# Kernel optimization log

Measured on AMD Instinct MI355X. Metric: run time of the kernel, lower is better.

Reference implementation:

```python
import jax, jax.numpy as jnp
import numpy as np
import math

N_HEADS = 16
ROPE_THETA = 10000.0


def _rope_cos_sin(seqlen, head_dim, theta=ROPE_THETA):
    # freqs_cis = polar(1, outer(t, 1/theta^(2i/d))) -> return cos, sin parts
    inv = 1.0 / (theta ** (jnp.arange(0, head_dim, 2, dtype=jnp.float32) / head_dim))
    t = jnp.arange(seqlen, dtype=jnp.float32)
    freqs = t[:, None] * inv[None, :]          # [S, hd/2]
    return jnp.cos(freqs), jnp.sin(freqs)


def _apply_rope(x, cos, sin):
    # x: [B, S, H, hd]; treat consecutive pairs as complex, rotate by e^{i*freq}
    B, S, H, hd = x.shape
    x2 = x.astype(jnp.float32).reshape(B, S, H, hd // 2, 2)
    xr, xi = x2[..., 0], x2[..., 1]
    c = cos[None, :, None, :]
    s = sin[None, :, None, :]
    out_r = xr * c - xi * s
    out_i = xr * s + xi * c
    return jnp.stack([out_r, out_i], axis=-1).reshape(B, S, H, hd).astype(x.dtype)


def setup_inputs() -> dict:
    key = jax.random.key(0)
    ks = jax.random.split(key, 5)
    dim = 2048
    B, S = 2, 2048
    scale = 1.0 / math.sqrt(dim)
    x = jax.random.normal(ks[0], (B, S, dim), dtype=jnp.float32)
    wq = jax.random.normal(ks[1], (dim, dim), dtype=jnp.float32) * scale
    wk = jax.random.normal(ks[2], (dim, dim), dtype=jnp.float32) * scale
    wv = jax.random.normal(ks[3], (dim, dim), dtype=jnp.float32) * scale
    wo = jax.random.normal(ks[4], (dim, dim), dtype=jnp.float32) * scale
    return {"x": x, "wq": wq, "wk": wk, "wv": wv, "wo": wo}


def reference(x, wq, wk, wv, wo):
    B, S, D = x.shape
    H = N_HEADS
    hd = D // H
    # nn.Linear(bias=False): y = x @ W.T
    q = (x @ wq.T).reshape(B, S, H, hd)
    k = (x @ wk.T).reshape(B, S, H, hd)
    v = (x @ wv.T).reshape(B, S, H, hd)
    cos, sin = _rope_cos_sin(S, hd)
    q = _apply_rope(q, cos, sin)
    k = _apply_rope(k, cos, sin)
    attn = jnp.einsum('bthd,bThd->bhtT', q, k) / jnp.sqrt(jnp.float32(hd))
    attn = jax.nn.softmax(attn, axis=-1)
    out = jnp.einsum('bhtT,bThd->bthd', attn, v).reshape(B, S, D)
    return out @ wo.T
```

## Files before the change

kernel.cpp:

```cpp
#include <hip/hip_runtime.h>
#include <math.h>

typedef unsigned short u16;
typedef __bf16 bf16x8 __attribute__((ext_vector_type(8)));
typedef short s16x4 __attribute__((ext_vector_type(4)));
typedef short s16x8 __attribute__((ext_vector_type(8)));
typedef float f32x4 __attribute__((ext_vector_type(4)));

#define B_ 2
#define S_ 2048
#define D_ 2048
#define H_ 16
#define HD_ 128
#define M_ 4096
#define N3_ 6144

#define AS1(p) ((__attribute__((address_space(1))) void*)(void*)(p))
#define AS3(p) ((__attribute__((address_space(3))) void*)(p))
#define GLD16(g, l) __builtin_amdgcn_global_load_lds(AS1(g), AS3(l), 16, 0, 0)

__device__ __forceinline__ u16 f2bf(float f) {
  unsigned u = __float_as_uint(f);
  return (u16)((u + 0x7FFFu + ((u >> 16) & 1u)) >> 16);
}
__device__ __forceinline__ float bf2f(u16 v) {
  return __uint_as_float(((unsigned)v) << 16);
}

__global__ void cvt5_k(const float* __restrict__ x, const float* __restrict__ wq,
                       const float* __restrict__ wk, const float* __restrict__ wv,
                       const float* __restrict__ wo, u16* __restrict__ xb,
                       u16* __restrict__ wqkvb, u16* __restrict__ wob) {
  int y = blockIdx.y;
  const float* s;
  u16* d;
  int n4;
  if (y == 0) {
    s = x; d = xb; n4 = M_ * D_ / 4;
  } else {
    s = (y == 1) ? wq : (y == 2) ? wk : (y == 3) ? wv : wo;
    d = (y == 4) ? wob : wqkvb + (size_t)(y - 1) * D_ * D_;
    n4 = D_ * D_ / 4;
  }
  int i = blockIdx.x * 256 + threadIdx.x;
  if (i >= n4) return;
  float4 v = ((const float4*)s)[i];
  ushort4 o;
  o.x = f2bf(v.x); o.y = f2bf(v.y); o.z = f2bf(v.z); o.w = f2bf(v.w);
  ((ushort4*)d)[i] = o;
}

__global__ void rope_tab_k(float2* __restrict__ tab) {
  int t = blockIdx.x * 256 + threadIdx.x;
  if (t >= S_ * 64) return;
  int s = t >> 6, i = t & 63;
  double inv = exp2(-(double)i * (13.287712379549449 / 64.0));
  double fr = (double)s * inv;
  double sv, cv;
  sincos(fr, &sv, &cv);
  tab[t] = make_float2((float)cv, (float)sv);
}

template <typename OT>
__global__ __launch_bounds__(512, 2) void gemm256_k(const u16* __restrict__ A,
                                                    const u16* __restrict__ B,
                                                    OT* __restrict__ C,
                                                    int M, int N, int K) {
  __shared__ alignas(16) u16 sm[65536];
  const int tid = threadIdx.x;
  const int wid = tid >> 6, lane = tid & 63;
  const int quad = lane >> 4, l16 = lane & 15;
  const int wr = wid >> 2, wc = wid & 3;

  const int nby = M >> 8, nbx = N >> 8, nwg = nbx * nby;
  int bid = blockIdx.x;
  int wg = (nwg % 8 == 0) ? (bid % 8) * (nwg >> 3) + (bid >> 3) : bid;
  const int m0 = (wg % nby) << 8, n0 = (wg / nby) << 8;

  const int rr = tid >> 3;
  const int sw8 = ((tid & 7) ^ (rr & 7)) * 8;
  const int gb0 = (rr & 31) + ((rr & 32) << 1);
  const u16* pA0_0 = A + (size_t)(m0 + rr) * K + sw8;
  const u16* pA0_1 = A + (size_t)(m0 + 128 + rr) * K + sw8;
  const u16* pA1_0 = A + (size_t)(m0 + 64 + rr) * K + sw8;
  const u16* pA1_1 = A + (size_t)(m0 + 192 + rr) * K + sw8;
  const u16* pB0_0 = B + (size_t)(n0 + gb0) * K + sw8;
  const u16* pB0_1 = B + (size_t)(n0 + 128 + gb0) * K + sw8;
  const u16* pB1_0 = B + (size_t)(n0 + 32 + gb0) * K + sw8;
  const u16* pB1_1 = B + (size_t)(n0 + 160 + gb0) * K + sw8;
  const int dst0 = wid * 64 * 8, dst1 = (512 + wid * 64) * 8;

  const int pj0 = (quad ^ (l16 & 7)) * 8;
  const int pj1 = ((4 + quad) ^ (l16 & 7)) * 8;

  f32x4 acc[8][4] = {};
  const int NT = K >> 6;

  GLD16(pA0_0, sm + dst0);
  GLD16(pA0_1, sm + dst1);
  GLD16(pB0_0, sm + 32768 + dst0);
  GLD16(pB0_1, sm + 32768 + dst1);
  GLD16(pB1_0, sm + 32768 + 8192 + dst0);
  GLD16(pB1_1, sm + 32768 + 8192 + dst1);
  GLD16(pA1_0, sm + 8192 + dst0);
  GLD16(pA1_1, sm + 8192 + dst1);
  asm volatile("s_waitcnt vmcnt(4)" ::: "memory");
  asm volatile("s_barrier" ::: "memory");

  int koff = 0;
#pragma unroll 1
  for (int t = 0; t < NT; ++t) {
    const int aB = (t & 1) * 16384, bB = 32768 + (t & 1) * 16384;
    const int aN = ((t + 1) & 1) * 16384, bN = 32768 + ((t + 1) & 1) * 16384;
    const bool pre = (t + 1 < NT);
    const int kn = koff + 64;
    bf16x8 a_[4][2], b_[4][2];

#pragma unroll
    for (int m = 0; m < 4; ++m) {
      int rb = aB + (wr * 64 + m * 16 + l16) * 64;
      a_[m][0] = *(const bf16x8*)&sm[rb + pj0];
      a_[m][1] = *(const bf16x8*)&sm[rb + pj1];
    }
#pragma unroll
    for (int n = 0; n < 2; ++n) {
      int rb = bB + (wc * 32 + n * 16 + l16) * 64;
      b_[n][0] = *(const bf16x8*)&sm[rb + pj0];
      b_[n][1] = *(const bf16x8*)&sm[rb + pj1];
    }
    if (pre) { GLD16(pA0_0 + kn, sm + aN + dst0); GLD16(pA0_1 + kn, sm + aN + dst1); }
    asm volatile("s_barrier" ::: "memory");
    __builtin_amdgcn_s_setprio(1);
#pragma unroll
    for (int m = 0; m < 4; ++m)
#pragma unroll
      for (int n = 0; n < 2; ++n) {
        acc[m][n] = __builtin_amdgcn_mfma_f32_16x16x32_bf16(a_[m][0], b_[n][0], acc[m][n], 0, 0, 0);
        acc[m][n] = __builtin_amdgcn_mfma_f32_16x16x32_bf16(a_[m][1], b_[n][1], acc[m][n], 0, 0, 0);
      }
    __builtin_amdgcn_s_setprio(0);
    if (pre) asm volatile("s_waitcnt vmcnt(4)" ::: "memory");
    else     asm volatile("s_waitcnt vmcnt(0)" ::: "memory");
    asm volatile("s_barrier" ::: "memory");

#pragma unroll
    for (int n = 0; n < 2; ++n) {
      int rb = bB + (128 + wc * 32 + n * 16 + l16) * 64;
      b_[2 + n][0] = *(const bf16x8*)&sm[rb + pj0];
      b_[2 + n][1] = *(const bf16x8*)&sm[rb + pj1];
    }
    if (pre) { GLD16(pB0_0 + kn, sm + bN + dst0); GLD16(pB0_1 + kn, sm + bN + dst1); }
    asm volatile("s_barrier" ::: "memory");
    __builtin_amdgcn_s_setprio(1);
#pragma unroll
    for (int m = 0; m < 4; ++m)
#pragma unroll
      for (int n = 0; n < 2; ++n) {
        acc[m][2 + n] = __builtin_amdgcn_mfma_f32_16x16x32_bf16(a_[m][0], b_[2 + n][0], acc[m][2 + n], 0, 0, 0);
        acc[m][2 + n] = __builtin_amdgcn_mfma_f32_16x16x32_bf16(a_[m][1], b_[2 + n][1], acc[m][2 + n], 0, 0, 0);
      }
    __builtin_amdgcn_s_setprio(0);
    if (pre) asm volatile("s_waitcnt vmcnt(4)" ::: "memory");
    else     asm volatile("s_waitcnt vmcnt(0)" ::: "memory");
    asm volatile("s_barrier" ::: "memory");

#pragma unroll
    for (int m = 0; m < 4; ++m) {
      int rb = aB + (128 + wr * 64 + m * 16 + l16) * 64;
      a_[m][0] = *(const bf16x8*)&sm[rb + pj0];
      a_[m][1] = *(const bf16x8*)&sm[rb + pj1];
    }
    if (pre) { GLD16(pB1_0 + kn, sm + bN + 8192 + dst0); GLD16(pB1_1 + kn, sm + bN + 8192 + dst1); }
    asm volatile("s_barrier" ::: "memory");
    __builtin_amdgcn_s_setprio(1);
#pragma unroll
    for (int m = 0; m < 4; ++m)
#pragma unroll
      for (int n = 0; n < 2; ++n) {
        acc[4 + m][n] = __builtin_amdgcn_mfma_f32_16x16x32_bf16(a_[m][0], b_[n][0], acc[4 + m][n], 0, 0, 0);
        acc[4 + m][n] = __builtin_amdgcn_mfma_f32_16x16x32_bf16(a_[m][1], b_[n][1], acc[4 + m][n], 0, 0, 0);
      }
    __builtin_amdgcn_s_setprio(0);
    asm volatile("s_barrier" ::: "memory");

    if (pre) { GLD16(pA1_0 + kn, sm + aN + 8192 + dst0); GLD16(pA1_1 + kn, sm + aN + 8192 + dst1); }
    asm volatile("s_barrier" ::: "memory");
    __builtin_amdgcn_s_setprio(1);
#pragma unroll
    for (int m = 0; m < 4; ++m)
#pragma unroll
      for (int n = 0; n < 2; ++n) {
        acc[4 + m][2 + n] = __builtin_amdgcn_mfma_f32_16x16x32_bf16(a_[m][0], b_[2 + n][0], acc[4 + m][2 + n], 0, 0, 0);
        acc[4 + m][2 + n] = __builtin_amdgcn_mfma_f32_16x16x32_bf16(a_[m][1], b_[2 + n][1], acc[4 + m][2 + n], 0, 0, 0);
      }
    __builtin_amdgcn_s_setprio(0);
    asm volatile("s_waitcnt vmcnt(4)" ::: "memory");
    asm volatile("s_barrier" ::: "memory");
    koff = kn;
  }

#pragma unroll
  for (int m = 0; m < 8; ++m) {
#pragma unroll
    for (int n = 0; n < 4; ++n) {
      int col = n0 + wc * 64 + n * 16 + l16;
#pragma unroll
      for (int r = 0; r < 4; ++r) {
        int row = m0 + wr * 128 + m * 16 + quad * 4 + r;
        if constexpr (sizeof(OT) == 4)
          C[(size_t)row * N + col] = acc[m][n][r];
        else
          C[(size_t)row * N + col] = f2bf(acc[m][n][r]);
      }
    }
  }
}

template <typename OT>
__global__ __launch_bounds__(256) void gemm_bt_k(const u16* __restrict__ A,
                                                 const u16* __restrict__ B,
                                                 OT* __restrict__ C,
                                                 int M, int N, int K) {
  __shared__ alignas(16) u16 As[128 * 32];
  __shared__ alignas(16) u16 Bs[128 * 32];
  const int tid = threadIdx.x;
  const int wave = tid >> 6, lane = tid & 63;
  const int quad = lane >> 4, l16 = lane & 15;
  const int m0 = blockIdx.y * 128, n0 = blockIdx.x * 128;
  const int wm = (wave >> 1) * 64, wn = (wave & 1) * 64;
  const u16* Ag = A + (size_t)m0 * K;
  const u16* Bg = B + (size_t)n0 * K;
  f32x4 acc[4][4] = {};
  const int c0 = tid, c1 = tid + 256;
  const int r0 = c0 >> 2, k0b = (c0 & 3) * 8;
  const int r1 = c1 >> 2, k1b = (c1 & 3) * 8;
  u16* la0 = As + (size_t)(wave * 64) * 8;
  u16* la1 = As + (size_t)(256 + wave * 64) * 8;
  u16* lb0 = Bs + (size_t)(wave * 64) * 8;
  u16* lb1 = Bs + (size_t)(256 + wave * 64) * 8;
  for (int kt = 0; kt < K; kt += 32) {
    GLD16(Ag + (size_t)r0 * K + kt + k0b, la0);
    GLD16(Ag + (size_t)r1 * K + kt + k1b, la1);
    GLD16(Bg + (size_t)r0 * K + kt + k0b, lb0);
    GLD16(Bg + (size_t)r1 * K + kt + k1b, lb1);
    __syncthreads();
    bf16x8 af[4], bfr[4];
#pragma unroll
    for (int i = 0; i < 4; ++i)
      af[i] = *(const bf16x8*)&As[(wm + i * 16 + l16) * 32 + quad * 8];
#pragma unroll
    for (int j = 0; j < 4; ++j)
      bfr[j] = *(const bf16x8*)&Bs[(wn + j * 16 + l16) * 32 + quad * 8];
#pragma unroll
    for (int i = 0; i < 4; ++i)
#pragma unroll
      for (int j = 0; j < 4; ++j)
        acc[i][j] = __builtin_amdgcn_mfma_f32_16x16x32_bf16(af[i], bfr[j], acc[i][j], 0, 0, 0);
    __syncthreads();
  }
#pragma unroll
  for (int i = 0; i < 4; ++i) {
#pragma unroll
    for (int j = 0; j < 4; ++j) {
      int n = n0 + wn + j * 16 + l16;
#pragma unroll
      for (int r = 0; r < 4; ++r) {
        int m = m0 + wm + i * 16 + quad * 4 + r;
        if constexpr (sizeof(OT) == 4)
          C[(size_t)m * N + n] = acc[i][j][r];
        else
          C[(size_t)m * N + n] = f2bf(acc[i][j][r]);
      }
    }
  }
}

__global__ void rope_k(const u16* __restrict__ qkv, const float2* __restrict__ tab,
                       u16* __restrict__ Qr, u16* __restrict__ Kr) {
  int t = blockIdx.x * 256 + threadIdx.x;
  int m = t >> 10;
  int h = (t >> 6) & 15;
  int i = t & 63;
  int s = m & (S_ - 1);
  int b = m >> 11;
  float2 cs = tab[(s << 6) | i];
  const u16* qp = qkv + (size_t)m * N3_ + h * HD_ + 2 * i;
  ushort2 qv = *(const ushort2*)qp;
  ushort2 kv = *(const ushort2*)(qp + D_);
  float qr = bf2f(qv.x), qi = bf2f(qv.y);
  float kr = bf2f(kv.x), ki = bf2f(kv.y);
  ushort2 qo, ko;
  qo.x = f2bf(qr * cs.x - qi * cs.y);
  qo.y = f2bf(qr * cs.y + qi * cs.x);
  ko.x = f2bf(kr * cs.x - ki * cs.y);
  ko.y = f2bf(kr * cs.y + ki * cs.x);
  size_t o = ((size_t)(b * H_ + h) * S_ + s) * HD_ + 2 * i;
  *(ushort2*)(Qr + o) = qo;
  *(ushort2*)(Kr + o) = ko;
}

__global__ __launch_bounds__(256) void vperm_k(const u16* __restrict__ qkv,
                                               u16* __restrict__ Vp) {
  int bh = blockIdx.y;
  int b = bh >> 4, h = bh & 15;
  int t = blockIdx.x * 256 + threadIdx.x;
  int d = t & 127, g = t >> 7;
  const u16* src = qkv + ((size_t)(b * S_ + 4 * g)) * N3_ + 2 * D_ + h * HD_ + d;
  ushort4 o;
  o.x = src[0];
  o.y = src[N3_];
  o.z = src[2 * N3_];
  o.w = src[3 * N3_];
  *(ushort4*)(Vp + (size_t)bh * S_ * HD_ + (size_t)t * 4) = o;
}

#if __has_builtin(__builtin_amdgcn_mfma_f32_16x16x16bf16_1k)
#define HAS_MFMA16 1
#endif

__global__ __launch_bounds__(256, 2) void flash_k(const u16* __restrict__ Q,
                                                  const u16* __restrict__ Kc,
                                                  const u16* __restrict__ Vp,
                                                  u16* __restrict__ O) {
  __shared__ alignas(16) u16 sm[32768];
  const int tid = threadIdx.x;
  const int wave = tid >> 6, lane = tid & 63;
  const int quad = lane >> 4, l16 = lane & 15;
  const int qt = blockIdx.x, bh = blockIdx.y;
  const int b = bh >> 4, h = bh & 15;
  const u16* vbase_g = Vp + (size_t)bh * S_ * HD_;

#pragma unroll
  for (int i = 0; i < 8; ++i) {
    int c = i * 256 + tid, row = c >> 4, jl = c & 15;
    int gj = (jl & 8) | ((jl ^ row) & 7);
    GLD16(Q + ((size_t)bh * S_ + qt * 128 + row) * HD_ + gj * 8,
          sm + (size_t)(i * 256 + wave * 64) * 8);
  }
#pragma unroll
  for (int i = 0; i < 4; ++i) {
    int c = i * 256 + tid, row = c >> 4, jl = c & 15;
    int gj = (jl & 8) | ((jl ^ row) & 7);
    GLD16(Kc + ((size_t)bh * S_ + row) * HD_ + gj * 8,
          sm + 16384 + (size_t)(i * 256 + wave * 64) * 8);
    GLD16(vbase_g + (size_t)(i * 256 + tid) * 8,
          sm + 24576 + (size_t)(i * 256 + wave * 64) * 8);
  }
  __syncthreads();

  bf16x8 qf[2][4];
#pragma unroll
  for (int qs = 0; qs < 2; ++qs) {
    int row = wave * 32 + qs * 16 + l16;
#pragma unroll
    for (int dk = 0; dk < 4; ++dk) {
      int c = dk * 4 + quad, pj = (c & 8) | ((c ^ row) & 7);
      qf[qs][dk] = *(const bf16x8*)&sm[row * 128 + pj * 8];
    }
  }
  __syncthreads();

  f32x4 acco[2][8] = {};
  f32x4 accl[2] = {};
  const float SCL = 0.08838834764831845f * 1.4426950408889634f;
#ifdef HAS_MFMA16
  const s16x4 ones = {(short)0x3F80, (short)0x3F80, (short)0x3F80, (short)0x3F80};
#else
  union { s16x8 s; bf16x8 b; } onesu;
  onesu.s = (s16x8){(short)0x3F80, (short)0x3F80, (short)0x3F80, (short)0x3F80,
                    (short)0x3F80, (short)0x3F80, (short)0x3F80, (short)0x3F80};
#endif

#pragma unroll 1
  for (int kt = 0; kt < 32; ++kt) {
    u16* cb = sm + ((kt & 1) ? 0 : 16384);
    u16* nb = sm + ((kt & 1) ? 16384 : 0);
    if (kt < 31) {
      const u16* vg = vbase_g + (size_t)(kt + 1) * 8192;
#pragma unroll
      for (int i = 0; i < 4; ++i) {
        int c = i * 256 + tid, row = c >> 4, jl = c & 15;
        int gj = (jl & 8) | ((jl ^ row) & 7);
        GLD16(Kc + ((size_t)bh * S_ + (kt + 1) * 64 + row) * HD_ + gj * 8,
              nb + (size_t)(i * 256 + wave * 64) * 8);
        GLD16(vg + (size_t)(i * 256 + tid) * 8,
              nb + 8192 + (size_t)(i * 256 + wave * 64) * 8);
      }
    }

    f32x4 sc[2][4] = {};
#pragma unroll
    for (int k4 = 0; k4 < 4; ++k4) {
      int row = k4 * 16 + l16;
#pragma unroll
      for (int dk = 0; dk < 4; ++dk) {
        int c = dk * 4 + quad, pj = (c & 8) | ((c ^ row) & 7);
        bf16x8 kf = *(const bf16x8*)&cb[row * 128 + pj * 8];
        sc[0][k4] = __builtin_amdgcn_mfma_f32_16x16x32_bf16(kf, qf[0][dk], sc[0][k4], 0, 0, 0);
        sc[1][k4] = __builtin_amdgcn_mfma_f32_16x16x32_bf16(kf, qf[1][dk], sc[1][k4], 0, 0, 0);
      }
    }

#ifdef HAS_MFMA16
    s16x4 ap[2][4];
#else
    bf16x8 ap[2][4];
#endif
#pragma unroll
    for (int qs = 0; qs < 2; ++qs) {
#pragma unroll
      for (int k4 = 0; k4 < 4; ++k4) {
        f32x4 s = sc[qs][k4];
        u16 p0 = f2bf(__builtin_amdgcn_exp2f(s[0] * SCL));
        u16 p1 = f2bf(__builtin_amdgcn_exp2f(s[1] * SCL));
        u16 p2 = f2bf(__builtin_amdgcn_exp2f(s[2] * SCL));
        u16 p3 = f2bf(__builtin_amdgcn_exp2f(s[3] * SCL));
#ifdef HAS_MFMA16
        ap[qs][k4] = (s16x4){(short)p0, (short)p1, (short)p2, (short)p3};
#else
        union { s16x8 s8; bf16x8 b8; } u;
        u.s8 = (s16x8){(short)p0, (short)p1, (short)p2, (short)p3, 0, 0, 0, 0};
        ap[qs][k4] = u.b8;
#endif
      }
    }

#pragma unroll
    for (int ck = 0; ck < 4; ++ck) {
      int vb = 8192 + (ck * 4 + quad) * 512 + l16 * 4;
#pragma unroll
      for (int df = 0; df < 8; ++df) {
        s16x4 bv = *(const s16x4*)&cb[vb + df * 64];
#ifdef HAS_MFMA16
        acco[0][df] = __builtin_amdgcn_mfma_f32_16x16x16bf16_1k(ap[0][ck], bv, acco[0][df], 0, 0, 0);
        acco[1][df] = __builtin_amdgcn_mfma_f32_16x16x16bf16_1k(ap[1][ck], bv, acco[1][df], 0, 0, 0);
#else
        union { s16x8 s8; bf16x8 b8; } vbu;
        vbu.s8 = (s16x8){bv[0], bv[1], bv[2], bv[3], 0, 0, 0, 0};
        acco[0][df] = __builtin_amdgcn_mfma_f32_16x16x32_bf16(ap[0][ck], vbu.b8, acco[0][df], 0, 0, 0);
        acco[1][df] = __builtin_amdgcn_mfma_f32_16x16x32_bf16(ap[1][ck], vbu.b8, acco[1][df], 0, 0, 0);
#endif
      }
#ifdef HAS_MFMA16
      accl[0] = __builtin_amdgcn_mfma_f32_16x16x16bf16_1k(ones, ap[0][ck], accl[0], 0, 0, 0);
      accl[1] = __builtin_amdgcn_mfma_f32_16x16x16bf16_1k(ones, ap[1][ck], accl[1], 0, 0, 0);
#else
      accl[0] = __builtin_amdgcn_mfma_f32_16x16x32_bf16(onesu.b, ap[0][ck], accl[0], 0, 0, 0);
      accl[1] = __builtin_amdgcn_mfma_f32_16x16x32_bf16(onesu.b, ap[1][ck], accl[1], 0, 0, 0);
#endif
    }
    __syncthreads();
  }

#pragma unroll
  for (int qs = 0; qs < 2; ++qs) {
    float lv = accl[qs][0];
    float linv[4];
#pragma unroll
    for (int r = 0; r < 4; ++r) linv[r] = 1.0f / __shfl(lv, quad * 4 + r);
    int rowb = qt * 128 + wave * 32 + qs * 16 + quad * 4;
#pragma unroll
    for (int df = 0; df < 8; ++df) {
      int col = h * HD_ + df * 16 + l16;
#pragma unroll
      for (int r = 0; r < 4; ++r)
        O[((size_t)(b * S_ + rowb + r)) * D_ + col] = f2bf(acco[qs][df][r] * linv[r]);
    }
  }
}

extern "C" void kernel_launch(void* const* d_in, const int* in_sizes, int n_in,
                              void* d_out, int out_size, void* d_ws, size_t ws_size,
                              hipStream_t stream) {
  const float* x  = (const float*)d_in[0];
  const float* wq = (const float*)d_in[1];
  const float* wk = (const float*)d_in[2];
  const float* wv = (const float*)d_in[3];
  const float* wo = (const float*)d_in[4];

  size_t off = 0;
  char* ws = (char*)d_ws;
  u16* xb    = (u16*)(ws + off); off += (size_t)M_ * D_ * 2;
  u16* wqkvb = (u16*)(ws + off); off += (size_t)3 * D_ * D_ * 2;
  u16* wob   = (u16*)(ws + off); off += (size_t)D_ * D_ * 2;
  u16* qkv   = (u16*)(ws + off); off += (size_t)M_ * N3_ * 2;
  u16* Qr    = (u16*)(ws + off); off += (size_t)M_ * D_ * 2;
  u16* Kr    = (u16*)(ws + off); off += (size_t)M_ * D_ * 2;
  u16* Vp    = (u16*)(ws + off); off += (size_t)M_ * D_ * 2;
  float2* tab = (float2*)(ws + off); off += (size_t)S_ * 64 * sizeof(float2);
  u16* Ob = qkv;
  if (off > ws_size) return;

  cvt5_k<<<dim3(M_ * D_ / 4 / 256, 5), 256, 0, stream>>>(x, wq, wk, wv, wo, xb, wqkvb, wob);
  rope_tab_k<<<(S_ * 64) / 256, 256, 0, stream>>>(tab);
  gemm256_k<u16><<<(M_ / 256) * (N3_ / 256), 512, 0, stream>>>(xb, wqkvb, qkv, M_, N3_, D_);
  rope_k<<<(M_ * H_ * 64) / 256, 256, 0, stream>>>(qkv, tab, Qr, Kr);
  vperm_k<<<dim3(S_ * HD_ / 4 / 256, B_ * H_), 256, 0, stream>>>(qkv, Vp);
  flash_k<<<dim3(S_ / 128, B_ * H_), 256, 0, stream>>>(Qr, Kr, Vp, Ob);
  gemm_bt_k<float><<<dim3(D_ / 128, M_ / 128), 256, 0, stream>>>(Ob, wob, (float*)d_out, M_, D_, D_);
}
```

Before: 418.2 us.

## Deepen GEMM global-to-LDS prefetch to two tiles ahead and remap block tiling

Restructures the 256x256 GEMM main loop so global_load_lds prefetches run two K-tiles ahead instead of one. The prologue now issues two tiles, and each iteration refills the buffer it just consumed, with vmcnt thresholds adjusted to match. It also adds a custom block-to-tile mapping for the 16x24 tile grid (the QKV projection shape), grouping 4x4 tile patches per XCD-stride group to improve L2 reuse. The deeper pipeline keeps more loads in flight but depends on the wait counts staying correct around buffer reuse.

After: 428.4 us. 1.02x slower.

```diff
diff --git a/kernel.cpp b/kernel.cpp
--- a/kernel.cpp
+++ b/kernel.cpp
@@ -74,8 +74,16 @@
 
   const int nby = M >> 8, nbx = N >> 8, nwg = nbx * nby;
   int bid = blockIdx.x;
-  int wg = (nwg % 8 == 0) ? (bid % 8) * (nwg >> 3) + (bid >> 3) : bid;
-  const int m0 = (wg % nby) << 8, n0 = (wg / nby) << 8;
+  int m0, n0;
+  if (nby == 16 && nbx == 24) {
+    int r = bid & 7, x = bid >> 3;
+    m0 = (((r & 3) << 2) + (x & 3)) << 8;
+    n0 = (((r >> 2) * 12) + (x >> 2)) << 8;
+  } else {
+    int wg = (nwg % 8 == 0) ? (bid % 8) * (nwg >> 3) + (bid >> 3) : bid;
+    m0 = (wg % nby) << 8;
+    n0 = (wg / nby) << 8;
+  }
 
   const int rr = tid >> 3;
   const int sw8 = ((tid & 7) ^ (rr & 7)) * 8;
@@ -96,24 +104,23 @@
   f32x4 acc[8][4] = {};
   const int NT = K >> 6;
 
-  GLD16(pA0_0, sm + dst0);
-  GLD16(pA0_1, sm + dst1);
-  GLD16(pB0_0, sm + 32768 + dst0);
-  GLD16(pB0_1, sm + 32768 + dst1);
-  GLD16(pB1_0, sm + 32768 + 8192 + dst0);
-  GLD16(pB1_1, sm + 32768 + 8192 + dst1);
-  GLD16(pA1_0, sm + 8192 + dst0);
-  GLD16(pA1_1, sm + 8192 + dst1);
-  asm volatile("s_waitcnt vmcnt(4)" ::: "memory");
+  GLD16(pB0_0, sm + 32768 + dst0); GLD16(pB0_1, sm + 32768 + dst1);
+  GLD16(pA0_0, sm + 0 + dst0);     GLD16(pA0_1, sm + 0 + dst1);
+  GLD16(pB1_0, sm + 40960 + dst0); GLD16(pB1_1, sm + 40960 + dst1);
+  GLD16(pA1_0, sm + 8192 + dst0);  GLD16(pA1_1, sm + 8192 + dst1);
+  GLD16(pB0_0 + 64, sm + 49152 + dst0); GLD16(pB0_1 + 64, sm + 49152 + dst1);
+  GLD16(pA0_0 + 64, sm + 16384 + dst0); GLD16(pA0_1 + 64, sm + 16384 + dst1);
+  GLD16(pB1_0 + 64, sm + 57344 + dst0); GLD16(pB1_1 + 64, sm + 57344 + dst1);
+  GLD16(pA1_0 + 64, sm + 24576 + dst0); GLD16(pA1_1 + 64, sm + 24576 + dst1);
+  asm volatile("s_waitcnt vmcnt(12)" ::: "memory");
   asm volatile("s_barrier" ::: "memory");
 
   int koff = 0;
 #pragma unroll 1
   for (int t = 0; t < NT; ++t) {
     const int aB = (t & 1) * 16384, bB = 32768 + (t & 1) * 16384;
-    const int aN = ((t + 1) & 1) * 16384, bN = 32768 + ((t + 1) & 1) * 16384;
-    const bool pre = (t + 1 < NT);
-    const int kn = koff + 64;
+    const bool pre = (t + 2 < NT);
+    const int kn2 = koff + 128;
     bf16x8 a_[4][2], b_[4][2];
 
 #pragma unroll
@@ -128,7 +135,6 @@
       b_[n][0] = *(const bf16x8*)&sm[rb + pj0];
       b_[n][1] = *(const bf16x8*)&sm[rb + pj1];
     }
-    if (pre) { GLD16(pA0_0 + kn, sm + aN + dst0); GLD16(pA0_1 + kn, sm + aN + dst1); }
     asm volatile("s_barrier" ::: "memory");
     __builtin_amdgcn_s_setprio(1);
 #pragma unroll
@@ -139,7 +145,7 @@
         acc[m][n] = __builtin_amdgcn_mfma_f32_16x16x32_bf16(a_[m][1], b_[n][1], acc[m][n], 0, 0, 0);
       }
     __builtin_amdgcn_s_setprio(0);
-    if (pre) asm volatile("s_waitcnt vmcnt(4)" ::: "memory");
+    if (pre) asm volatile("s_waitcnt vmcnt(10)" ::: "memory");
     else     asm volatile("s_waitcnt vmcnt(0)" ::: "memory");
     asm volatile("s_barrier" ::: "memory");
 
@@ -149,7 +155,7 @@
       b_[2 + n][0] = *(const bf16x8*)&sm[rb + pj0];
       b_[2 + n][1] = *(const bf16x8*)&sm[rb + pj1];
     }
-    if (pre) { GLD16(pB0_0 + kn, sm + bN + dst0); GLD16(pB0_1 + kn, sm + bN + dst1); }
+    if (pre) { GLD16(pB0_0 + kn2, sm + bB + dst0); GLD16(pB0_1 + kn2, sm + bB + dst1); }
     asm volatile("s_barrier" ::: "memory");
     __builtin_amdgcn_s_setprio(1);
 #pragma unroll
@@ -160,7 +166,7 @@
         acc[m][2 + n] = __builtin_amdgcn_mfma_f32_16x16x32_bf16(a_[m][1], b_[2 + n][1], acc[m][2 + n], 0, 0, 0);
       }
     __builtin_amdgcn_s_setprio(0);
-    if (pre) asm volatile("s_waitcnt vmcnt(4)" ::: "memory");
+    if (pre) asm volatile("s_waitcnt vmcnt(10)" ::: "memory");
     else     asm volatile("s_waitcnt vmcnt(0)" ::: "memory");
     asm volatile("s_barrier" ::: "memory");
 
@@ -170,7 +176,10 @@
       a_[m][0] = *(const bf16x8*)&sm[rb + pj0];
       a_[m][1] = *(const bf16x8*)&sm[rb + pj1];
     }
-    if (pre) { GLD16(pB1_0 + kn, sm + bN + 8192 + dst0); GLD16(pB1_1 + kn, sm + bN + 8192 + dst1); }
+    if (pre) {
+      GLD16(pA0_0 + kn2, sm + aB + dst0);        GLD16(pA0_1 + kn2, sm + aB + dst1);
+      GLD16(pB1_0 + kn2, sm + bB + 8192 + dst0); GLD16(pB1_1 + kn2, sm + bB + 8192 + dst1);
+    }
     asm volatile("s_barrier" ::: "memory");
     __builtin_amdgcn_s_setprio(1);
 #pragma unroll
@@ -183,7 +192,7 @@
     __builtin_amdgcn_s_setprio(0);
     asm volatile("s_barrier" ::: "memory");
 
-    if (pre) { GLD16(pA1_0 + kn, sm + aN + 8192 + dst0); GLD16(pA1_1 + kn, sm + aN + 8192 + dst1); }
+    if (pre) { GLD16(pA1_0 + kn2, sm + aB + 8192 + dst0); GLD16(pA1_1 + kn2, sm + aB + 8192 + dst1); }
     asm volatile("s_barrier" ::: "memory");
     __builtin_amdgcn_s_setprio(1);
 #pragma unroll
@@ -194,9 +203,10 @@
         acc[4 + m][2 + n] = __builtin_amdgcn_mfma_f32_16x16x32_bf16(a_[m][1], b_[2 + n][1], acc[4 + m][2 + n], 0, 0, 0);
       }
     __builtin_amdgcn_s_setprio(0);
-    asm volatile("s_waitcnt vmcnt(4)" ::: "memory");
-    asm volatile("s_barrier" ::: "memory");
-    koff = kn;
+    if (pre) asm volatile("s_waitcnt vmcnt(12)" ::: "memory");
+    else     asm volatile("s_waitcnt vmcnt(0)" ::: "memory");
+    asm volatile("s_barrier" ::: "memory");
+    koff += 64;
   }
 
 #pragma unroll
```

## Fuse RoPE and V permutation into QKV GEMM epilogue

Applied to the files above, without the earlier changes.

The QKV projection GEMM now writes its results straight into the rotated Q/K head-major buffers and the permuted V layout, so the separate rope and vperm kernels and the intermediate qkv buffer go away. The rotation partner is fetched with a lane shuffle, since adjacent columns sit in adjacent lanes, and cos/sin come from the precomputed table. This removes a full round trip of the M×3D bf16 intermediate through memory plus two launches. In exchange the epilogue does scattered 2-byte stores and per-element table loads, which may coalesce worse than the original row-major stores.

Result: slower. 443.7 us (+6.1%).

```diff
diff --git a/kernel.cpp b/kernel.cpp
--- a/kernel.cpp
+++ b/kernel.cpp
@@ -61,20 +61,22 @@
   tab[t] = make_float2((float)cv, (float)sv);
 }
 
-template <typename OT>
-__global__ __launch_bounds__(512, 2) void gemm256_k(const u16* __restrict__ A,
-                                                    const u16* __restrict__ B,
-                                                    OT* __restrict__ C,
-                                                    int M, int N, int K) {
+__global__ __launch_bounds__(512, 2) void gemm256_rope_k(const u16* __restrict__ A,
+                                                         const u16* __restrict__ B,
+                                                         const float2* __restrict__ tab,
+                                                         u16* __restrict__ Qr,
+                                                         u16* __restrict__ Kr,
+                                                         u16* __restrict__ Vp) {
   __shared__ alignas(16) u16 sm[65536];
   const int tid = threadIdx.x;
   const int wid = tid >> 6, lane = tid & 63;
   const int quad = lane >> 4, l16 = lane & 15;
   const int wr = wid >> 2, wc = wid & 3;
-
-  const int nby = M >> 8, nbx = N >> 8, nwg = nbx * nby;
+  const int K = D_;
+
+  const int nby = M_ >> 8;
   int bid = blockIdx.x;
-  int wg = (nwg % 8 == 0) ? (bid % 8) * (nwg >> 3) + (bid >> 3) : bid;
+  int wg = (bid & 7) * 48 + (bid >> 3);
   const int m0 = (wg % nby) << 8, n0 = (wg / nby) << 8;
 
   const int rr = tid >> 3;
@@ -199,18 +201,29 @@
     koff = kn;
   }
 
+  const int third = n0 >> 11;
+  u16* OutQK = (third == 0) ? Qr : Kr;
 #pragma unroll
   for (int m = 0; m < 8; ++m) {
 #pragma unroll
     for (int n = 0; n < 4; ++n) {
       int col = n0 + wc * 64 + n * 16 + l16;
+      int d = col & 127;
+      int h = (col >> 7) & 15;
 #pragma unroll
       for (int r = 0; r < 4; ++r) {
         int row = m0 + wr * 128 + m * 16 + quad * 4 + r;
-        if constexpr (sizeof(OT) == 4)
-          C[(size_t)row * N + col] = acc[m][n][r];
-        else
-          C[(size_t)row * N + col] = f2bf(acc[m][n][r]);
+        int s = row & (S_ - 1);
+        int b = row >> 11;
+        float v = acc[m][n][r];
+        if (third < 2) {
+          float p = __shfl_xor(v, 1);
+          float2 cs = tab[(s << 6) | (d >> 1)];
+          float o = (d & 1) ? (p * cs.y + v * cs.x) : (v * cs.x - p * cs.y);
+          OutQK[((size_t)((b * H_ + h) * S_ + s)) * HD_ + d] = f2bf(o);
+        } else {
+          Vp[(size_t)(b * H_ + h) * (S_ * HD_) + (size_t)(s >> 2) * 512 + d * 4 + (s & 3)] = f2bf(v);
+        }
       }
     }
   }
@@ -275,45 +288,6 @@
   }
 }
 
-__global__ void rope_k(const u16* __restrict__ qkv, const float2* __restrict__ tab,
-                       u16* __restrict__ Qr, u16* __restrict__ Kr) {
-  int t = blockIdx.x * 256 + threadIdx.x;
-  int m = t >> 10;
-  int h = (t >> 6) & 15;
-  int i = t & 63;
-  int s = m & (S_ - 1);
-  int b = m >> 11;
-  float2 cs = tab[(s << 6) | i];
-  const u16* qp = qkv + (size_t)m * N3_ + h * HD_ + 2 * i;
-  ushort2 qv = *(const ushort2*)qp;
-  ushort2 kv = *(const ushort2*)(qp + D_);
-  float qr = bf2f(qv.x), qi = bf2f(qv.y);
-  float kr = bf2f(kv.x), ki = bf2f(kv.y);
-  ushort2 qo, ko;
-  qo.x = f2bf(qr * cs.x - qi * cs.y);
-  qo.y = f2bf(qr * cs.y + qi * cs.x);
-  ko.x = f2bf(kr * cs.x - ki * cs.y);
-  ko.y = f2bf(kr * cs.y + ki * cs.x);
-  size_t o = ((size_t)(b * H_ + h) * S_ + s) * HD_ + 2 * i;
-  *(ushort2*)(Qr + o) = qo;
-  *(ushort2*)(Kr + o) = ko;
-}
-
-__global__ __launch_bounds__(256) void vperm_k(const u16* __restrict__ qkv,
-                                               u16* __restrict__ Vp) {
-  int bh = blockIdx.y;
-  int b = bh >> 4, h = bh & 15;
-  int t = blockIdx.x * 256 + threadIdx.x;
-  int d = t & 127, g = t >> 7;
-  const u16* src = qkv + ((size_t)(b * S_ + 4 * g)) * N3_ + 2 * D_ + h * HD_ + d;
-  ushort4 o;
-  o.x = src[0];
-  o.y = src[N3_];
-  o.z = src[2 * N3_];
-  o.w = src[3 * N3_];
-  *(ushort4*)(Vp + (size_t)bh * S_ * HD_ + (size_t)t * 4) = o;
-}
-
 #if __has_builtin(__builtin_amdgcn_mfma_f32_16x16x16bf16_1k)
 #define HAS_MFMA16 1
 #endif
@@ -483,19 +457,16 @@
   u16* xb    = (u16*)(ws + off); off += (size_t)M_ * D_ * 2;
   u16* wqkvb = (u16*)(ws + off); off += (size_t)3 * D_ * D_ * 2;
   u16* wob   = (u16*)(ws + off); off += (size_t)D_ * D_ * 2;
-  u16* qkv   = (u16*)(ws + off); off += (size_t)M_ * N3_ * 2;
+  u16* Ob    = (u16*)(ws + off); off += (size_t)M_ * D_ * 2;
   u16* Qr    = (u16*)(ws + off); off += (size_t)M_ * D_ * 2;
   u16* Kr    = (u16*)(ws + off); off += (size_t)M_ * D_ * 2;
   u16* Vp    = (u16*)(ws + off); off += (size_t)M_ * D_ * 2;
   float2* tab = (float2*)(ws + off); off += (size_t)S_ * 64 * sizeof(float2);
-  u16* Ob = qkv;
   if (off > ws_size) return;
 
   cvt5_k<<<dim3(M_ * D_ / 4 / 256, 5), 256, 0, stream>>>(x, wq, wk, wv, wo, xb, wqkvb, wob);
   rope_tab_k<<<(S_ * 64) / 256, 256, 0, stream>>>(tab);
-  gemm256_k<u16><<<(M_ / 256) * (N3_ / 256), 512, 0, stream>>>(xb, wqkvb, qkv, M_, N3_, D_);
-  rope_k<<<(M_ * H_ * 64) / 256, 256, 0, stream>>>(qkv, tab, Qr, Kr);
-  vperm_k<<<dim3(S_ * HD_ / 4 / 256, B_ * H_), 256, 0, stream>>>(qkv, Vp);
+  gemm256_rope_k<<<(M_ / 256) * (N3_ / 256), 512, 0, stream>>>(xb, wqkvb, tab, Qr, Kr, Vp);
   flash_k<<<dim3(S_ / 128, B_ * H_), 256, 0, stream>>>(Qr, Kr, Vp, Ob);
   gemm_bt_k<float><<<dim3(D_ / 128, M_ / 128), 256, 0, stream>>>(Ob, wob, (float*)d_out, M_, D_, D_);
 }
```
